# Kernel tuning notes

Hardware: AMD Instinct MI355X
Metric: run time of the kernel (lower is better)

## Reference

```python
import jax, jax.numpy as jnp
import numpy as np

S, B, I, H = 2048, 128, 128, 128


def setup_inputs() -> dict:
    key = jax.random.key(0)
    k1, k2, k3, k4, k5 = jax.random.split(key, 5)
    x = jax.random.normal(k1, (S, B, I), dtype=jnp.float32)
    V = jax.random.normal(k2, (4 * H, I), dtype=jnp.float32) * 0.05
    W = jax.random.normal(k3, (4 * H, H), dtype=jnp.float32) * 0.05
    b = jax.random.normal(k4, (4 * H,), dtype=jnp.float32) * 0.05
    b2 = jax.random.normal(k5, (4 * H,), dtype=jnp.float32) * 0.05
    return {"x": x, "V": V, "W": W, "b": b, "b2": b2}


def reference(x, V, W, b, b2):
    seq_len, batch, _ = x.shape
    hid = W.shape[1]
    # Precompute input contribution for all timesteps (same math, batched matmul)
    xg = jnp.einsum('sbi,gi->sbg', x, V) + b + b2  # (S, B, 4H)

    def step(carry, xg_t):
        h, c = carry
        gates = xg_t + h @ W.T  # (B, 4H)
        i, f, g, o = jnp.split(gates, 4, axis=1)
        i = jax.nn.sigmoid(i)
        f = jax.nn.sigmoid(f)
        g = jnp.tanh(g)
        o = jax.nn.sigmoid(o)
        c = f * c + i * g
        h = o * jnp.tanh(c)
        return (h, c), h

    h0 = jnp.zeros((batch, hid), dtype=x.dtype)
    c0 = jnp.zeros((batch, hid), dtype=x.dtype)
    (h_T, c_T), hs = jax.lax.scan(step, (h0, c0), xg)  # hs: (S, B, H)
    # Original torch.cat of h_t.unsqueeze(1) along dim 0 -> (S*B, 1, H)
    h_seq = hs.reshape(seq_len * batch, 1, hid)
    return h_seq, h_T[:, None, :], c_T[:, None, :]
```

## Files before the change

### kernel.cpp

```cpp
#include <hip/hip_runtime.h>
#include <hip/hip_bf16.h>
#include <hip/hip_fp16.h>


#define S_LEN 2048
#define BATCH 128
#define HID   128
#define G4    512

typedef _Float16 h2_t __attribute__((ext_vector_type(2)));
typedef _Float16 h8_t __attribute__((ext_vector_type(8)));
typedef float    f4_t __attribute__((ext_vector_type(4)));

__global__ __launch_bounds__(256, 2)
void xg_gemm(const float* __restrict__ x, const float* __restrict__ V,
             const float* __restrict__ b, const float* __restrict__ b2,
             __half* __restrict__ xg)
{
    __shared__ h8_t As[128 * 16];
    __shared__ h8_t Bs[128 * 16];

    const int t  = threadIdx.x;
    const int m0 = blockIdx.y * 128;
    const int n0 = blockIdx.x * 128;

#pragma unroll
    for (int r = 0; r < 8; ++r) {
        int id  = t + 256 * r;
        int row = id >> 4;
        int j   = id & 15;
        const float4* gx = (const float4*)(x + (long)(m0 + row) * 128 + j * 8);
        float4 a0 = gx[0], a1 = gx[1];
        h8_t ha = { (_Float16)a0.x, (_Float16)a0.y, (_Float16)a0.z, (_Float16)a0.w,
                    (_Float16)a1.x, (_Float16)a1.y, (_Float16)a1.z, (_Float16)a1.w };
        As[row * 16 + (j ^ (row & 15))] = ha;
        const float4* gv = (const float4*)(V + (long)(n0 + row) * 128 + j * 8);
        float4 b0 = gv[0], b1 = gv[1];
        h8_t hb = { (_Float16)b0.x, (_Float16)b0.y, (_Float16)b0.z, (_Float16)b0.w,
                    (_Float16)b1.x, (_Float16)b1.y, (_Float16)b1.z, (_Float16)b1.w };
        Bs[row * 16 + (j ^ (row & 15))] = hb;
    }
    __syncthreads();

    const int w    = t >> 6;
    const int lane = t & 63;
    const int m    = lane & 15;
    const int quad = lane >> 4;

    f4_t acc[2][8];
#pragma unroll
    for (int i = 0; i < 2; ++i)
#pragma unroll
        for (int j = 0; j < 8; ++j) acc[i][j] = (f4_t)0.f;

#pragma unroll
    for (int ks = 0; ks < 4; ++ks) {
        int ch = ks * 4 + quad;
        h8_t a0 = As[(w * 32      + m) * 16 + (ch ^ m)];
        h8_t a1 = As[(w * 32 + 16 + m) * 16 + (ch ^ m)];
#pragma unroll
        for (int nt = 0; nt < 8; ++nt) {
            h8_t bf = Bs[(nt * 16 + m) * 16 + (ch ^ m)];
            acc[0][nt] = __builtin_amdgcn_mfma_f32_16x16x32_f16(a0, bf, acc[0][nt], 0, 0, 0);
            acc[1][nt] = __builtin_amdgcn_mfma_f32_16x16x32_f16(a1, bf, acc[1][nt], 0, 0, 0);
        }
    }

#pragma unroll
    for (int nt = 0; nt < 8; ++nt) {
        int col = n0 + nt * 16 + m;
        float bias = b[col] + b2[col];
#pragma unroll
        for (int mi = 0; mi < 2; ++mi) {
#pragma unroll
            for (int rg = 0; rg < 4; ++rg) {
                long mrow = (long)(m0 + w * 32 + mi * 16 + quad * 4 + rg);
                xg[mrow * G4 + col] = __float2half(acc[mi][nt][rg] + bias);
            }
        }
    }
}

__device__ __forceinline__ float fsig(float x) {
    return __builtin_amdgcn_rcpf(1.f + __expf(-x));
}
__device__ __forceinline__ float ftanh(float x) {
    return 1.f - 2.f * __builtin_amdgcn_rcpf(1.f + __expf(2.f * x));
}
__device__ __forceinline__ void bar() {
    asm volatile("s_waitcnt lgkmcnt(0)" ::: "memory");
    __builtin_amdgcn_s_barrier();
    asm volatile("" ::: "memory");
}

__global__ __launch_bounds__(512, 2)
void lstm_scan(const __half* __restrict__ xg, const float* __restrict__ W,
               float* __restrict__ out)
{
    const int bidx = blockIdx.x;
    const int t    = threadIdx.x;
    const int w    = t >> 6;
    const int lane = t & 63;
    const int col  = lane & 15;
    const int quad = lane >> 4;
    const int rg   = col & 3;
    const int hid  = 16 * w + quad * 4 + rg;

    __shared__ __align__(16) __half h_buf[2][HID];

    h8_t a[4][4];
#pragma unroll
    for (int g = 0; g < 4; ++g) {
        const float* Wr = W + (long)(g * 128 + 16 * w + col) * 128 + quad * 8;
#pragma unroll
        for (int kc = 0; kc < 4; ++kc) {
            const float4* wp = (const float4*)(Wr + kc * 32);
            float4 v0 = wp[0], v1 = wp[1];
            a[g][kc] = h8_t{ (_Float16)v0.x, (_Float16)v0.y, (_Float16)v0.z, (_Float16)v0.w,
                             (_Float16)v1.x, (_Float16)v1.y, (_Float16)v1.z, (_Float16)v1.w };
        }
    }

    if (t < HID) h_buf[0][t] = __float2half(0.f);
    __syncthreads();

    const __half* xp = xg + (long)bidx * G4 + hid;
    const long step_stride = (long)BATCH * G4;

    __half p0[4], p1[4];
#pragma unroll
    for (int g = 0; g < 4; ++g) {
        p0[g] = xp[g * 128];
        p1[g] = xp[step_stride + g * 128];
    }

    float c = 0.f, hlast = 0.f;
    float* out_h = out + (long)bidx * HID;
    const long SBH = (long)S_LEN * BATCH * HID;

    const bool sel1 = (col & 1) != 0;
    const bool sel2 = (col & 2) != 0;

    for (int s = 0; s < S_LEN; ++s) {
        long soff = (long)((s + 2 < S_LEN) ? s + 2 : S_LEN - 1) * step_stride;
        __half nx[4];
#pragma unroll
        for (int g = 0; g < 4; ++g) nx[g] = xp[soff + g * 128];

        const h8_t* hb = (const h8_t*)(&h_buf[s & 1][0]);

        f4_t acc0 = (f4_t)0.f, acc1 = (f4_t)0.f, acc2 = (f4_t)0.f, acc3 = (f4_t)0.f;
#pragma unroll
        for (int kc = 0; kc < 4; ++kc) {
            h8_t bf = hb[kc * 4 + quad];
            acc0 = __builtin_amdgcn_mfma_f32_16x16x32_f16(a[0][kc], bf, acc0, 0, 0, 0);
            acc1 = __builtin_amdgcn_mfma_f32_16x16x32_f16(a[1][kc], bf, acc1, 0, 0, 0);
            acc2 = __builtin_amdgcn_mfma_f32_16x16x32_f16(a[2][kc], bf, acc2, 0, 0, 0);
            acc3 = __builtin_amdgcn_mfma_f32_16x16x32_f16(a[3][kc], bf, acc3, 0, 0, 0);
        }

        float v01, v23;
        v01 = sel1 ? acc0[1] : acc0[0];  v23 = sel1 ? acc0[3] : acc0[2];
        float pi = (sel2 ? v23 : v01) + __half2float(p0[0]);
        v01 = sel1 ? acc1[1] : acc1[0];  v23 = sel1 ? acc1[3] : acc1[2];
        float pf = (sel2 ? v23 : v01) + __half2float(p0[1]);
        v01 = sel1 ? acc2[1] : acc2[0];  v23 = sel1 ? acc2[3] : acc2[2];
        float pg = (sel2 ? v23 : v01) + __half2float(p0[2]);
        v01 = sel1 ? acc3[1] : acc3[0];  v23 = sel1 ? acc3[3] : acc3[2];
        float po = (sel2 ? v23 : v01) + __half2float(p0[3]);

        float ia = fsig(pi);
        float fa = fsig(pf);
        float ga = ftanh(pg);
        float oa = fsig(po);
        c = fa * c + ia * ga;
        float hv = oa * ftanh(c);
        hlast = hv;

        if (col < 4) {
            h_buf[(s + 1) & 1][hid] = __float2half(hv);
            out_h[(long)s * (BATCH * HID) + hid] = hv;
        }
        bar();

#pragma unroll
        for (int g = 0; g < 4; ++g) { p0[g] = p1[g]; p1[g] = nx[g]; }
    }

    if (col < 4) {
        out[SBH + (long)bidx * HID + hid]                     = hlast;
        out[SBH + (long)BATCH * HID + (long)bidx * HID + hid] = c;
    }
}

extern "C" void kernel_launch(void* const* d_in, const int* in_sizes, int n_in,
                              void* d_out, int out_size, void* d_ws, size_t ws_size,
                              hipStream_t stream) {
    const float* x  = (const float*)d_in[0];
    const float* V  = (const float*)d_in[1];
    const float* W  = (const float*)d_in[2];
    const float* b  = (const float*)d_in[3];
    const float* b2 = (const float*)d_in[4];
    float* out = (float*)d_out;
    __half* xg = (__half*)d_ws;

    dim3 g1(G4 / 128, (S_LEN * BATCH) / 128);
    xg_gemm<<<g1, dim3(256), 0, stream>>>(x, V, b, b2, xg);
    lstm_scan<<<dim3(BATCH), dim3(512), 0, stream>>>(xg, W, out);
}
```

Before: 1.449 ms.

## Fuse input projection into LSTM scan, computing next step's x·V during recurrence

Drops the separate xg GEMM kernel and its fp16 xg workspace. x is now only converted to fp16, and each scan block holds V fragments in registers, computing the input-gate contribution for step s+1 with MFMAs while step s runs, in a software-pipelined pair of steps. This removes the write and re-read of the S×B×4H intermediate, which cuts memory traffic to about a quarter. In exchange it doubles the register-resident weights and adds 16 MFMAs per step inside the latency-critical recurrence, which may raise register pressure and occupancy risk.

```diff
diff --git a/kernel.cpp b/kernel.cpp
--- a/kernel.cpp
+++ b/kernel.cpp
@@ -8,77 +8,20 @@
 #define HID   128
 #define G4    512
 
-typedef _Float16 h2_t __attribute__((ext_vector_type(2)));
 typedef _Float16 h8_t __attribute__((ext_vector_type(8)));
 typedef float    f4_t __attribute__((ext_vector_type(4)));
 
-__global__ __launch_bounds__(256, 2)
-void xg_gemm(const float* __restrict__ x, const float* __restrict__ V,
-             const float* __restrict__ b, const float* __restrict__ b2,
-             __half* __restrict__ xg)
+#define MFMA16(A, B, C) __builtin_amdgcn_mfma_f32_16x16x32_f16((A), (B), (C), 0, 0, 0)
+
+__global__ __launch_bounds__(256)
+void x_cvt(const float* __restrict__ x, __half* __restrict__ x16)
 {
-    __shared__ h8_t As[128 * 16];
-    __shared__ h8_t Bs[128 * 16];
-
-    const int t  = threadIdx.x;
-    const int m0 = blockIdx.y * 128;
-    const int n0 = blockIdx.x * 128;
-
-#pragma unroll
-    for (int r = 0; r < 8; ++r) {
-        int id  = t + 256 * r;
-        int row = id >> 4;
-        int j   = id & 15;
-        const float4* gx = (const float4*)(x + (long)(m0 + row) * 128 + j * 8);
-        float4 a0 = gx[0], a1 = gx[1];
-        h8_t ha = { (_Float16)a0.x, (_Float16)a0.y, (_Float16)a0.z, (_Float16)a0.w,
-                    (_Float16)a1.x, (_Float16)a1.y, (_Float16)a1.z, (_Float16)a1.w };
-        As[row * 16 + (j ^ (row & 15))] = ha;
-        const float4* gv = (const float4*)(V + (long)(n0 + row) * 128 + j * 8);
-        float4 b0 = gv[0], b1 = gv[1];
-        h8_t hb = { (_Float16)b0.x, (_Float16)b0.y, (_Float16)b0.z, (_Float16)b0.w,
-                    (_Float16)b1.x, (_Float16)b1.y, (_Float16)b1.z, (_Float16)b1.w };
-        Bs[row * 16 + (j ^ (row & 15))] = hb;
-    }
-    __syncthreads();
-
-    const int w    = t >> 6;
-    const int lane = t & 63;
-    const int m    = lane & 15;
-    const int quad = lane >> 4;
-
-    f4_t acc[2][8];
-#pragma unroll
-    for (int i = 0; i < 2; ++i)
-#pragma unroll
-        for (int j = 0; j < 8; ++j) acc[i][j] = (f4_t)0.f;
-
-#pragma unroll
-    for (int ks = 0; ks < 4; ++ks) {
-        int ch = ks * 4 + quad;
-        h8_t a0 = As[(w * 32      + m) * 16 + (ch ^ m)];
-        h8_t a1 = As[(w * 32 + 16 + m) * 16 + (ch ^ m)];
-#pragma unroll
-        for (int nt = 0; nt < 8; ++nt) {
-            h8_t bf = Bs[(nt * 16 + m) * 16 + (ch ^ m)];
-            acc[0][nt] = __builtin_amdgcn_mfma_f32_16x16x32_f16(a0, bf, acc[0][nt], 0, 0, 0);
-            acc[1][nt] = __builtin_amdgcn_mfma_f32_16x16x32_f16(a1, bf, acc[1][nt], 0, 0, 0);
-        }
-    }
-
-#pragma unroll
-    for (int nt = 0; nt < 8; ++nt) {
-        int col = n0 + nt * 16 + m;
-        float bias = b[col] + b2[col];
-#pragma unroll
-        for (int mi = 0; mi < 2; ++mi) {
-#pragma unroll
-            for (int rg = 0; rg < 4; ++rg) {
-                long mrow = (long)(m0 + w * 32 + mi * 16 + quad * 4 + rg);
-                xg[mrow * G4 + col] = __float2half(acc[mi][nt][rg] + bias);
-            }
-        }
-    }
+    long i = ((long)blockIdx.x * 256 + threadIdx.x) * 8;
+    const float4* p = (const float4*)(x + i);
+    float4 v0 = p[0], v1 = p[1];
+    h8_t h = { (_Float16)v0.x, (_Float16)v0.y, (_Float16)v0.z, (_Float16)v0.w,
+               (_Float16)v1.x, (_Float16)v1.y, (_Float16)v1.z, (_Float16)v1.w };
+    *(h8_t*)((_Float16*)x16 + i) = h;
 }
 
 __device__ __forceinline__ float fsig(float x) {
@@ -93,9 +36,77 @@
     asm volatile("" ::: "memory");
 }
 
+#define LSTEP(S, XUSE, XBLD, XF, SN)                                           \
+    {                                                                          \
+        const int s = (S);                                                     \
+        const h8_t* hb = (const h8_t*)(&h_buf[s & 1][0]);                      \
+        h8_t hf0 = hb[quad], hf1 = hb[4 + quad], hf2 = hb[8 + quad],           \
+             hf3 = hb[12 + quad];                                              \
+        f4_t g0 = XUSE[0], g1 = XUSE[1], g2 = XUSE[2], g3 = XUSE[3];           \
+        g0 = MFMA16(a[0][0], hf0, g0);  g1 = MFMA16(a[1][0], hf0, g1);         \
+        g2 = MFMA16(a[2][0], hf0, g2);  g3 = MFMA16(a[3][0], hf0, g3);         \
+        g0 = MFMA16(a[0][1], hf1, g0);  g1 = MFMA16(a[1][1], hf1, g1);         \
+        g2 = MFMA16(a[2][1], hf1, g2);  g3 = MFMA16(a[3][1], hf1, g3);         \
+        g0 = MFMA16(a[0][2], hf2, g0);  g1 = MFMA16(a[1][2], hf2, g1);         \
+        g2 = MFMA16(a[2][2], hf2, g2);  g3 = MFMA16(a[3][2], hf2, g3);         \
+        g0 = MFMA16(a[0][3], hf3, g0);  g1 = MFMA16(a[1][3], hf3, g1);         \
+        g2 = MFMA16(a[2][3], hf3, g2);  g3 = MFMA16(a[3][3], hf3, g3);         \
+                         \
+        XBLD[0] = (f4_t)0.f; XBLD[1] = (f4_t)0.f;                              \
+        XBLD[2] = (f4_t)0.f; XBLD[3] = (f4_t)0.f;                              \
+        XBLD[0] = MFMA16(va[0][0], XF[0], XBLD[0]);                            \
+        XBLD[1] = MFMA16(va[1][0], XF[0], XBLD[1]);                            \
+        XBLD[2] = MFMA16(va[2][0], XF[0], XBLD[2]);                            \
+        XBLD[3] = MFMA16(va[3][0], XF[0], XBLD[3]);                            \
+        XBLD[0] = MFMA16(va[0][1], XF[1], XBLD[0]);                            \
+        XBLD[1] = MFMA16(va[1][1], XF[1], XBLD[1]);                            \
+        XBLD[2] = MFMA16(va[2][1], XF[1], XBLD[2]);                            \
+        XBLD[3] = MFMA16(va[3][1], XF[1], XBLD[3]);                            \
+        XBLD[0] = MFMA16(va[0][2], XF[2], XBLD[0]);                            \
+        XBLD[1] = MFMA16(va[1][2], XF[2], XBLD[1]);                            \
+        XBLD[2] = MFMA16(va[2][2], XF[2], XBLD[2]);                            \
+        XBLD[3] = MFMA16(va[3][2], XF[2], XBLD[3]);                            \
+        XBLD[0] = MFMA16(va[0][3], XF[3], XBLD[0]);                            \
+        XBLD[1] = MFMA16(va[1][3], XF[3], XBLD[1]);                            \
+        XBLD[2] = MFMA16(va[2][3], XF[3], XBLD[2]);                            \
+        XBLD[3] = MFMA16(va[3][3], XF[3], XBLD[3]);                            \
+                    \
+        {                                                                      \
+            const _Float16* q = (const _Float16*)xp + (long)(SN) * xstep;      \
+            XF[0] = *(const h8_t*)(q);                                         \
+            XF[1] = *(const h8_t*)(q + 32);                                    \
+            XF[2] = *(const h8_t*)(q + 64);                                    \
+            XF[3] = *(const h8_t*)(q + 96);                                    \
+        }                                                                      \
+                     \
+        float v01, v23;                                                        \
+        v01 = sel1 ? g0[1] : g0[0];  v23 = sel1 ? g0[3] : g0[2];               \
+        float pi = (sel2 ? v23 : v01) + bias[0];                               \
+        v01 = sel1 ? g1[1] : g1[0];  v23 = sel1 ? g1[3] : g1[2];               \
+        float pf = (sel2 ? v23 : v01) + bias[1];                               \
+        v01 = sel1 ? g2[1] : g2[0];  v23 = sel1 ? g2[3] : g2[2];               \
+        float pg = (sel2 ? v23 : v01) + bias[2];                               \
+        v01 = sel1 ? g3[1] : g3[0];  v23 = sel1 ? g3[3] : g3[2];               \
+        float po = (sel2 ? v23 : v01) + bias[3];                               \
+        float ia = fsig(pi);                                                   \
+        float fa = fsig(pf);                                                   \
+        float ga = ftanh(pg);                                                  \
+        float oa = fsig(po);                                                   \
+        c = fa * c + ia * ga;                                                  \
+        float hv = oa * ftanh(c);                                              \
+        hlast = hv;                                                            \
+        if (col < 4) {                                                         \
+            h_buf[(s + 1) & 1][hid] = __float2half(hv);                        \
+            *outp = hv;                                                        \
+        }                                                                      \
+        outp += BATCH * HID;                                                   \
+        bar();                                                                 \
+    }
+
 __global__ __launch_bounds__(512, 2)
-void lstm_scan(const __half* __restrict__ xg, const float* __restrict__ W,
-               float* __restrict__ out)
+void lstm_scan(const __half* __restrict__ x16, const float* __restrict__ W,
+               const float* __restrict__ V, const float* __restrict__ b,
+               const float* __restrict__ b2, float* __restrict__ out)
 {
     const int bidx = blockIdx.x;
     const int t    = threadIdx.x;
@@ -108,83 +119,67 @@
 
     __shared__ __align__(16) __half h_buf[2][HID];
 
-    h8_t a[4][4];
+    h8_t a[4][4], va[4][4];
 #pragma unroll
     for (int g = 0; g < 4; ++g) {
         const float* Wr = W + (long)(g * 128 + 16 * w + col) * 128 + quad * 8;
+        const float* Vr = V + (long)(g * 128 + 16 * w + col) * 128 + quad * 8;
 #pragma unroll
         for (int kc = 0; kc < 4; ++kc) {
             const float4* wp = (const float4*)(Wr + kc * 32);
-            float4 v0 = wp[0], v1 = wp[1];
-            a[g][kc] = h8_t{ (_Float16)v0.x, (_Float16)v0.y, (_Float16)v0.z, (_Float16)v0.w,
-                             (_Float16)v1.x, (_Float16)v1.y, (_Float16)v1.z, (_Float16)v1.w };
+            float4 w0 = wp[0], w1 = wp[1];
+            a[g][kc] = h8_t{ (_Float16)w0.x, (_Float16)w0.y, (_Float16)w0.z, (_Float16)w0.w,
+                             (_Float16)w1.x, (_Float16)w1.y, (_Float16)w1.z, (_Float16)w1.w };
+            const float4* vp = (const float4*)(Vr + kc * 32);
+            float4 u0 = vp[0], u1 = vp[1];
+            va[g][kc] = h8_t{ (_Float16)u0.x, (_Float16)u0.y, (_Float16)u0.z, (_Float16)u0.w,
+                              (_Float16)u1.x, (_Float16)u1.y, (_Float16)u1.z, (_Float16)u1.w };
         }
     }
+
+    float bias[4];
+#pragma unroll
+    for (int g = 0; g < 4; ++g)
+        bias[g] = b[g * 128 + hid] + b2[g * 128 + hid];
 
     if (t < HID) h_buf[0][t] = __float2half(0.f);
     __syncthreads();
 
-    const __half* xp = xg + (long)bidx * G4 + hid;
-    const long step_stride = (long)BATCH * G4;
-
-    __half p0[4], p1[4];
-#pragma unroll
-    for (int g = 0; g < 4; ++g) {
-        p0[g] = xp[g * 128];
-        p1[g] = xp[step_stride + g * 128];
-    }
+    const _Float16* xp = (const _Float16*)x16 + (long)bidx * 128 + quad * 8;
+    const long xstep = (long)BATCH * 128;
+
+    h8_t xfE[4], xfO[4];
+#pragma unroll
+    for (int kc = 0; kc < 4; ++kc) {
+        xfE[kc] = *(const h8_t*)(xp + kc * 32);
+        xfO[kc] = *(const h8_t*)(xp + xstep + kc * 32);
+    }
+
+    f4_t xA[4], xB[4];
+#pragma unroll
+    for (int g = 0; g < 4; ++g) xA[g] = (f4_t)0.f;
+#pragma unroll
+    for (int kc = 0; kc < 4; ++kc) {
+        xA[0] = MFMA16(va[0][kc], xfE[kc], xA[0]);
+        xA[1] = MFMA16(va[1][kc], xfE[kc], xA[1]);
+        xA[2] = MFMA16(va[2][kc], xfE[kc], xA[2]);
+        xA[3] = MFMA16(va[3][kc], xfE[kc], xA[3]);
+    }
+#pragma unroll
+    for (int kc = 0; kc < 4; ++kc)
+        xfE[kc] = *(const h8_t*)(xp + 2 * xstep + kc * 32);
 
     float c = 0.f, hlast = 0.f;
-    float* out_h = out + (long)bidx * HID;
+    float* outp = out + (long)bidx * HID + hid;
     const long SBH = (long)S_LEN * BATCH * HID;
-
     const bool sel1 = (col & 1) != 0;
     const bool sel2 = (col & 2) != 0;
 
-    for (int s = 0; s < S_LEN; ++s) {
-        long soff = (long)((s + 2 < S_LEN) ? s + 2 : S_LEN - 1) * step_stride;
-        __half nx[4];
-#pragma unroll
-        for (int g = 0; g < 4; ++g) nx[g] = xp[soff + g * 128];
-
-        const h8_t* hb = (const h8_t*)(&h_buf[s & 1][0]);
-
-        f4_t acc0 = (f4_t)0.f, acc1 = (f4_t)0.f, acc2 = (f4_t)0.f, acc3 = (f4_t)0.f;
-#pragma unroll
-        for (int kc = 0; kc < 4; ++kc) {
-            h8_t bf = hb[kc * 4 + quad];
-            acc0 = __builtin_amdgcn_mfma_f32_16x16x32_f16(a[0][kc], bf, acc0, 0, 0, 0);
-            acc1 = __builtin_amdgcn_mfma_f32_16x16x32_f16(a[1][kc], bf, acc1, 0, 0, 0);
-            acc2 = __builtin_amdgcn_mfma_f32_16x16x32_f16(a[2][kc], bf, acc2, 0, 0, 0);
-            acc3 = __builtin_amdgcn_mfma_f32_16x16x32_f16(a[3][kc], bf, acc3, 0, 0, 0);
-        }
-
-        float v01, v23;
-        v01 = sel1 ? acc0[1] : acc0[0];  v23 = sel1 ? acc0[3] : acc0[2];
-        float pi = (sel2 ? v23 : v01) + __half2float(p0[0]);
-        v01 = sel1 ? acc1[1] : acc1[0];  v23 = sel1 ? acc1[3] : acc1[2];
-        float pf = (sel2 ? v23 : v01) + __half2float(p0[1]);
-        v01 = sel1 ? acc2[1] : acc2[0];  v23 = sel1 ? acc2[3] : acc2[2];
-        float pg = (sel2 ? v23 : v01) + __half2float(p0[2]);
-        v01 = sel1 ? acc3[1] : acc3[0];  v23 = sel1 ? acc3[3] : acc3[2];
-        float po = (sel2 ? v23 : v01) + __half2float(p0[3]);
-
-        float ia = fsig(pi);
-        float fa = fsig(pf);
-        float ga = ftanh(pg);
-        float oa = fsig(po);
-        c = fa * c + ia * ga;
-        float hv = oa * ftanh(c);
-        hlast = hv;
-
-        if (col < 4) {
-            h_buf[(s + 1) & 1][hid] = __float2half(hv);
-            out_h[(long)s * (BATCH * HID) + hid] = hv;
-        }
-        bar();
-
-#pragma unroll
-        for (int g = 0; g < 4; ++g) { p0[g] = p1[g]; p1[g] = nx[g]; }
+    for (int s0 = 0; s0 < S_LEN; s0 += 2) {
+        int sn0 = s0 + 3; if (sn0 > S_LEN - 1) sn0 = S_LEN - 1;
+        LSTEP(s0,     xA, xB, xfO, sn0);
+        int sn1 = s0 + 4; if (sn1 > S_LEN - 1) sn1 = S_LEN - 1;
+        LSTEP(s0 + 1, xB, xA, xfE, sn1);
     }
 
     if (col < 4) {
@@ -202,9 +197,8 @@
     const float* b  = (const float*)d_in[3];
     const float* b2 = (const float*)d_in[4];
     float* out = (float*)d_out;
-    __half* xg = (__half*)d_ws;
-
-    dim3 g1(G4 / 128, (S_LEN * BATCH) / 128);
-    xg_gemm<<<g1, dim3(256), 0, stream>>>(x, V, b, b2, xg);
-    lstm_scan<<<dim3(BATCH), dim3(512), 0, stream>>>(xg, W, out);
-}
+    __half* x16 = (__half*)d_ws;
+
+    x_cvt<<<dim3(16384), dim3(256), 0, stream>>>(x, x16);
+    lstm_scan<<<dim3(BATCH), dim3(512), 0, stream>>>(x16, W, V, b, b2, out);
+}
```

After: 1.607 ms. +10.9%, slower.
